# Kernel optimization log

Hardware: AMD Instinct MI355X
Metric: run time of the kernel (lower is better)

## Reference

```python
import jax, jax.numpy as jnp
import numpy as np

B, S, D, A = 8, 4096, 128, 128


def _pos_encoding(seq_len, dim):
    # sin/cos positional encoding, same construction as the torch buffer
    pos = np.arange(seq_len, dtype=np.float32)[:, None]
    div = np.exp(np.arange(0, dim, 2, dtype=np.float32) * (-np.log(10000.0) / dim))
    pe = np.zeros((seq_len, dim), dtype=np.float32)
    pe[:, 0::2] = np.sin(pos * div)
    pe[:, 1::2] = np.cos(pos * div)
    return jnp.asarray(pe)


def setup_inputs() -> dict:
    key = jax.random.key(0)
    ks = jax.random.split(key, 7)
    sc = 1.0 / np.sqrt(D)
    return {
        "x": jax.random.normal(ks[0], (B, S, D), dtype=jnp.float32),
        "Wq": jax.random.normal(ks[1], (D, A), dtype=jnp.float32) * sc,
        "bq": jnp.zeros((A,), dtype=jnp.float32),
        "Wk": jax.random.normal(ks[2], (D, A), dtype=jnp.float32) * sc,
        "bk": jnp.zeros((A,), dtype=jnp.float32),
        "Wv": jax.random.normal(ks[3], (D, A), dtype=jnp.float32) * sc,
        "bv": jnp.zeros((A,), dtype=jnp.float32),
    }


def reference(x, Wq, bq, Wk, bk, Wv, bv):
    b, s, d = x.shape
    pe = _pos_encoding(s, d)  # [S, D]
    xp = x + pe[None]  # broadcast add of positional encoding
    q = xp @ Wq + bq  # [B, S, A]
    k = xp @ Wk + bk
    v = xp @ Wv + bv
    scale = 1.0 / jnp.sqrt(jnp.asarray(Wq.shape[1], dtype=jnp.float32))
    scores = jnp.einsum("bsa,bta->bst", q, k) * scale  # [B, S, S]
    weights = jax.nn.softmax(scores, axis=-1)
    out = jnp.einsum("bst,bta->bsa", weights, v)  # [B, S, A]
    return out
```

## Files before the change

kernel.cpp:

```cpp
#include <hip/hip_runtime.h>

#define BB 8
#define SS 4096
#define DD 128

typedef __attribute__((ext_vector_type(8))) short v8s;
typedef __attribute__((ext_vector_type(4))) float v4f;
typedef __attribute__((ext_vector_type(16))) float v16f;

__device__ __forceinline__ unsigned short f2bf(float f) {
    unsigned int u = __float_as_uint(f);
    u += 0x7fffu + ((u >> 16) & 1u);
    return (unsigned short)(u >> 16);
}
__device__ __forceinline__ unsigned int pk_bf16(float a, float b) {
    unsigned int ua = __float_as_uint(a) + 0x8000u;
    unsigned int ub = __float_as_uint(b) + 0x8000u;
    return __builtin_amdgcn_perm(ub, ua, 0x07060302u);
}

#if !defined(__HIP_DEVICE_COMPILE__)
#define MFMA16(a, b, c) (c)
#define MFMA32(a, b, c) (c)
#define GLDS16(g, l)
#define WAITVM(n)
#define WAITLGKM()
#define BAR()
#else
#define MFMA16(a, b, c) __builtin_amdgcn_mfma_f32_16x16x32_bf16((a), (b), (c), 0, 0, 0)
#define MFMA32(a, b, c) __builtin_amdgcn_mfma_f32_32x32x16_bf16((a), (b), (c), 0, 0, 0)
#define GLDS16(g, l)                                                         \
    __builtin_amdgcn_global_load_lds(                                        \
        (const __attribute__((address_space(1))) unsigned int*)(g),          \
        (__attribute__((address_space(3))) unsigned int*)(l), 16, 0, 0)
#define WAITVM(n) asm volatile("s_waitcnt vmcnt(" #n ")" ::: "memory")
#define WAITLGKM() asm volatile("s_waitcnt lgkmcnt(0)" ::: "memory")
#define BAR()                                                                \
    do {                                                                     \
        asm volatile("" ::: "memory");                                       \
        __builtin_amdgcn_s_barrier();                                        \
        __builtin_amdgcn_sched_barrier(0);                                   \
        asm volatile("" ::: "memory");                                       \
    } while (0)
#endif

#if !defined(__HIP_DEVICE_COMPILE__)
#define EXP2F(x) exp2f(x)
#elif __has_builtin(__builtin_amdgcn_exp2f)
#define EXP2F(x) __builtin_amdgcn_exp2f(x)
#else
#define EXP2F(x) exp2f(x)
#endif

#define QSCALE 0.12751743f

__global__ __launch_bounds__(256) void prep_kernel(
    const float* __restrict__ Wq, const float* __restrict__ Wk,
    const float* __restrict__ Wv, unsigned short* __restrict__ Wt)
{
    int id = blockIdx.x * 256 + threadIdx.x;
    int w = id >> 14;
    int n = (id >> 7) & 127;
    int k = id & 127;
    const float* W = (w == 0) ? Wq : (w == 1) ? Wk : Wv;
    Wt[id] = f2bf(W[k * 128 + n]);
}

__global__ __launch_bounds__(256, 3) void proj_kernel(
    const float* __restrict__ x, const unsigned short* __restrict__ Wt,
    const float* __restrict__ bq, const float* __restrict__ bk,
    const float* __restrict__ bv,
    unsigned short* __restrict__ qo, unsigned short* __restrict__ ko,
    unsigned short* __restrict__ vo)
{
    __shared__ __attribute__((aligned(16))) unsigned short w_lds[128 * 136];
    __shared__ __attribute__((aligned(16))) unsigned short o_lds[9216];

    const int tid = threadIdx.x;
    const int wave = tid >> 6;
    const int lane = tid & 63;
    const int quad = lane >> 4;
    const int l15 = lane & 15;
    const int bid = blockIdx.x;
    const int mat = bid % 3;
    const int rbase = (bid / 3) * 64;

    const unsigned short* Wp = Wt + (mat << 14);
#pragma unroll
    for (int it = 0; it < 8; ++it) {
        int id = it * 256 + tid;
        int n = id >> 4, c8 = id & 15;
        *(v8s*)(w_lds + n * 136 + c8 * 8) = *(const v8s*)(Wp + n * 128 + c8 * 8);
    }

    const int flatrow = rbase + wave * 16 + l15;
    const int srow = flatrow & 4095;
    v8s af[4];
#pragma unroll
    for (int kc = 0; kc < 4; ++kc) {
        const int kbase = kc * 32 + quad * 8;
        const v4f* xp = (const v4f*)(x + (size_t)flatrow * DD + kbase);
        v4f x0 = xp[0], x1 = xp[1];
        float p[8];
#pragma unroll
        for (int j = 0; j < 8; j += 2) {
            float freq = __expf((float)(kbase + j) * -0.07195578415606394f);
            float arg = (float)srow * freq;
            p[j] = __sinf(arg);
            p[j + 1] = __cosf(arg);
        }
        v8s a;
#pragma unroll
        for (int j = 0; j < 4; ++j) a[j] = (short)f2bf(x0[j] + p[j]);
#pragma unroll
        for (int j = 0; j < 4; ++j) a[4 + j] = (short)f2bf(x1[j] + p[4 + j]);
        af[kc] = a;
    }

    const float* bias = (mat == 0) ? bq : (mat == 1) ? bk : bv;
    const int quadp = ((quad & 1) << 1) | (quad >> 1);
    __syncthreads();

#pragma unroll
    for (int nb = 0; nb < 8; ++nb) {
        const int col = nb * 16 + l15;
        v4f acc = {0.f, 0.f, 0.f, 0.f};
#pragma unroll
        for (int kc = 0; kc < 4; ++kc) {
            v8s bf = *(const v8s*)(w_lds + col * 136 + kc * 32 + quad * 8);
            acc = MFMA16(af[kc], bf, acc);
        }
        float bval = bias[col];
#pragma unroll
        for (int reg = 0; reg < 4; ++reg) {
            float val = acc[reg] + bval;
            if (mat == 0) {
                int lr = wave * 16 + quad * 4 + reg;
                o_lds[lr * 136 + col] = f2bf(val * QSCALE);
            } else if (mat == 1) {
                int lr = wave * 16 + quad * 4 + reg;
                o_lds[lr * 136 + col] = f2bf(val);
            } else {
                int plr = wave * 16 + quadp * 4 + reg;
                o_lds[col * 72 + plr] = f2bf(val);
            }
        }
    }
    __syncthreads();

    if (mat <= 1) {
        unsigned short* outp = (mat == 0) ? qo : ko;
#pragma unroll
        for (int it = 0; it < 4; ++it) {
            int id = it * 256 + tid;
            int r = id >> 4, c8 = id & 15;
            *(v8s*)(outp + (size_t)(rbase + r) * DD + c8 * 8) =
                *(const v8s*)(o_lds + r * 136 + c8 * 8);
        }
    } else {
        const int b0 = rbase >> 12, s0 = rbase & 4095;
#pragma unroll
        for (int it = 0; it < 4; ++it) {
            int id = it * 256 + tid;
            int a = id >> 3, c = id & 7;
            *(v8s*)(vo + ((size_t)(b0 * 128 + a)) * SS + s0 + c * 8) =
                *(const v8s*)(o_lds + a * 72 + c * 8);
        }
    }
}

#define HKEYS 2048
#define NT 32
__global__ __launch_bounds__(512, 2) void flash_kernel(
    const unsigned short* __restrict__ qp,
    const unsigned short* __restrict__ kp,
    const unsigned short* __restrict__ vp,
    float* __restrict__ outp)
{
    __shared__ __attribute__((aligned(16))) unsigned short k_lds[2][2][8192];
    __shared__ __attribute__((aligned(16))) unsigned short v_lds[2][2][8192];
    __shared__ float xl[8][32];

    const int tid = threadIdx.x;
    const int wave = tid >> 6;
    const int lane = tid & 63;
    const int hi = lane >> 5;
    const int l31 = lane & 31;
    const int half = wave >> 2;
    const int qs = wave & 3;
    const int wv = wave & 3;
    const int bid = blockIdx.x;
    const int b = bid & 7;
    const int qt = bid >> 3;
    const int qbase = qt * 128;

    const size_t qrow = (size_t)(b * SS + qbase + qs * 32 + l31) * DD;
    v8s qf[8];
#pragma unroll
    for (int kc = 0; kc < 8; ++kc)
        qf[kc] = *(const v8s*)(qp + qrow + kc * 16 + hi * 8);

    v16f o[4];
#pragma unroll
    for (int fg = 0; fg < 4; ++fg)
#pragma unroll
        for (int r = 0; r < 16; ++r) o[fg][r] = 0.f;
    float lp = 0.f;

    const int kro = half * 32768 + l31 * 256 + ((hi ^ (l31 & 15)) << 4);
    const int vro = half * 32768 + l31 * 128 + (((l31 & 7) ^ hi) << 4);

    const int krow = wv * 4 + (lane >> 4);
    const unsigned short* ksrc =
        kp + ((size_t)(b * SS + half * HKEYS) + krow) * DD +
        (((lane & 15) ^ krow) << 3);
    const int vrow = lane >> 3;
    const unsigned short* vsrc =
        vp + (size_t)b * DD * SS + (size_t)(wv * 8 + vrow) * SS + half * HKEYS +
        (((lane & 7) ^ vrow) << 3);
    unsigned short* kd0 = &k_lds[half][0][wv * 512];
    unsigned short* vd0 = &v_lds[half][0][wv * 512];

    auto stage = [&](int p, int t) {
        unsigned short* kd = kd0 + p * 8192;
        unsigned short* vd = vd0 + p * 8192;
        const unsigned short* ks = ksrc + (size_t)t * 64 * DD;
        const unsigned short* vs = vsrc + t * 64;
#pragma unroll
        for (int it = 0; it < 4; ++it)
            GLDS16(ks + (size_t)it * 16 * DD, kd + it * 2048);
#pragma unroll
        for (int it = 0; it < 4; ++it)
            GLDS16(vs + (size_t)it * 32 * SS, vd + it * 2048);
    };

    auto compute = [&](int p, int sub) {
        const int ka = kro + p * 16384 + sub * 8192;
        v16f s;
#pragma unroll
        for (int r = 0; r < 16; ++r) s[r] = 0.f;
#pragma unroll
        for (int kc = 0; kc < 8; ++kc) {
            v8s af = *(const v8s*)((const char*)k_lds + (ka ^ (kc << 5)));
            s = MFMA32(af, qf[kc], s);
        }
        float e[16];
#pragma unroll
        for (int r = 0; r < 16; ++r) e[r] = EXP2F(s[r]);
        lp += (((e[0] + e[1]) + (e[2] + e[3])) + ((e[4] + e[5]) + (e[6] + e[7]))) +
              (((e[8] + e[9]) + (e[10] + e[11])) + ((e[12] + e[13]) + (e[14] + e[15])));
        union { v8s v[2]; unsigned int u[8]; } P;
#pragma unroll
        for (int g = 0; g < 2; ++g)
#pragma unroll
            for (int m = 0; m < 4; ++m)
                P.u[g * 4 + m] = pk_bf16(e[2 * m + 8 * g], e[2 * m + 8 * g + 1]);
        const int vb2 = (vro + p * 16384) ^ (sub << 6);
#pragma unroll
        for (int g = 0; g < 2; ++g) {
            const int vg = vb2 ^ (g << 5);
#pragma unroll
            for (int fg = 0; fg < 4; ++fg) {
                v8s bf = *(const v8s*)((const char*)v_lds + (vg + fg * 4096));
                o[fg] = MFMA32(P.v[g], bf, o[fg]);
            }
        }
    };

    stage(0, 0);
#pragma unroll 1
    for (int t = 0; t < NT; t += 2) {
        stage(1, t + 1);
        WAITVM(8);
        BAR();
        compute(0, 0);
        compute(0, 1);
        WAITLGKM();
        BAR();
        if (t + 2 < NT) {
            stage(0, t + 2);
            WAITVM(8);
        } else {
            WAITVM(0);
        }
        BAR();
        compute(1, 0);
        compute(1, 1);
        WAITLGKM();
        BAR();
    }

    lp += __shfl_xor(lp, 32);
    if (hi == 0) xl[wave][l31] = lp;

    float* kf = (float*)&k_lds[0][0][0];

    auto putO = [&](float* base) {
#pragma unroll
        for (int fg = 0; fg < 4; ++fg) {
            v4f* bp = (v4f*)(base + fg * 1024 + lane * 16);
#pragma unroll
            for (int c = 0; c < 4; ++c) {
                v4f tv = {o[fg][c * 4 + 0], o[fg][c * 4 + 1],
                          o[fg][c * 4 + 2], o[fg][c * 4 + 3]};
                bp[c ^ (lane & 3)] = tv;
            }
        }
    };
    auto addO = [&](const float* base) {
#pragma unroll
        for (int fg = 0; fg < 4; ++fg) {
            const v4f* bp = (const v4f*)(base + fg * 1024 + lane * 16);
#pragma unroll
            for (int c = 0; c < 4; ++c) {
                v4f tv = bp[c ^ (lane & 3)];
#pragma unroll
                for (int j = 0; j < 4; ++j) o[fg][c * 4 + j] += tv[j];
            }
        }
    };

    if (half == 1) putO(kf + qs * 4096);
    __syncthreads();
    if (half == 0) {
        addO(kf + qs * 4096);
        float ir[16];
#pragma unroll
        for (int r = 0; r < 16; ++r) {
            int qr = (r & 3) + 8 * (r >> 2) + 4 * hi;
            ir[r] = 1.0f / (xl[qs][qr] + xl[4 + qs][qr]);
        }
#pragma unroll
        for (int fg = 0; fg < 4; ++fg)
#pragma unroll
            for (int r = 0; r < 16; ++r) {
                int qr = (r & 3) + 8 * (r >> 2) + 4 * hi;
                outp[(size_t)(b * SS + qbase + qs * 32 + qr) * DD +
                     fg * 32 + l31] = o[fg][r] * ir[r];
            }
    }
}

extern "C" void kernel_launch(void* const* d_in, const int* in_sizes, int n_in,
                              void* d_out, int out_size, void* d_ws, size_t ws_size,
                              hipStream_t stream)
{
    const float* x  = (const float*)d_in[0];
    const float* Wq = (const float*)d_in[1];
    const float* bq = (const float*)d_in[2];
    const float* Wk = (const float*)d_in[3];
    const float* bk = (const float*)d_in[4];
    const float* Wv = (const float*)d_in[5];
    const float* bv = (const float*)d_in[6];
    float* out = (float*)d_out;

    unsigned short* Wt = (unsigned short*)d_ws;
    unsigned short* q  = Wt + 49152;
    unsigned short* k  = q + (size_t)BB * SS * DD;
    unsigned short* vT = k + (size_t)BB * SS * DD;

    hipLaunchKernelGGL(prep_kernel, dim3(192), dim3(256), 0, stream,
                       Wq, Wk, Wv, Wt);
    hipLaunchKernelGGL(proj_kernel, dim3(BB * SS / 64 * 3), dim3(256), 0, stream,
                       x, Wt, bq, bk, bv, q, k, vT);
    hipLaunchKernelGGL(flash_kernel, dim3(BB * SS / 128), dim3(512), 0, stream,
                       q, k, vT, out);
}
```

Measured before the change: 167.8 us.

## Store V in MFMA fragment layout and load it straight into registers

The projection kernel now computes Q, K and V in one block per 64 rows, looping over the three weight matrices. This avoids recomputing the positional-encoded input three times. V is written in a fragment-native layout so the flash kernel can load each lane's B operand directly from global memory into registers, double-buffered as X and Y. That removes the V LDS staging and its LDS reads. The cost is more vector registers and global-load latency exposed inside the compute loop, and the projection kernel runs with lower occupancy.

```diff
diff --git a/kernel.cpp b/kernel.cpp
--- a/kernel.cpp
+++ b/kernel.cpp
@@ -66,12 +66,12 @@
     Wt[id] = f2bf(W[k * 128 + n]);
 }
 
-__global__ __launch_bounds__(256, 3) void proj_kernel(
+__global__ __launch_bounds__(256, 2) void proj_kernel(
     const float* __restrict__ x, const unsigned short* __restrict__ Wt,
     const float* __restrict__ bq, const float* __restrict__ bk,
     const float* __restrict__ bv,
     unsigned short* __restrict__ qo, unsigned short* __restrict__ ko,
-    unsigned short* __restrict__ vo)
+    unsigned short* __restrict__ vF)
 {
     __shared__ __attribute__((aligned(16))) unsigned short w_lds[128 * 136];
     __shared__ __attribute__((aligned(16))) unsigned short o_lds[9216];
@@ -81,17 +81,7 @@
     const int lane = tid & 63;
     const int quad = lane >> 4;
     const int l15 = lane & 15;
-    const int bid = blockIdx.x;
-    const int mat = bid % 3;
-    const int rbase = (bid / 3) * 64;
-
-    const unsigned short* Wp = Wt + (mat << 14);
-#pragma unroll
-    for (int it = 0; it < 8; ++it) {
-        int id = it * 256 + tid;
-        int n = id >> 4, c8 = id & 15;
-        *(v8s*)(w_lds + n * 136 + c8 * 8) = *(const v8s*)(Wp + n * 128 + c8 * 8);
-    }
+    const int rbase = blockIdx.x * 64;
 
     const int flatrow = rbase + wave * 16 + l15;
     const int srow = flatrow & 4095;
@@ -117,54 +107,67 @@
         af[kc] = a;
     }
 
-    const float* bias = (mat == 0) ? bq : (mat == 1) ? bk : bv;
     const int quadp = ((quad & 1) << 1) | (quad >> 1);
-    __syncthreads();
-
-#pragma unroll
-    for (int nb = 0; nb < 8; ++nb) {
-        const int col = nb * 16 + l15;
-        v4f acc = {0.f, 0.f, 0.f, 0.f};
-#pragma unroll
-        for (int kc = 0; kc < 4; ++kc) {
-            v8s bf = *(const v8s*)(w_lds + col * 136 + kc * 32 + quad * 8);
-            acc = MFMA16(af[kc], bf, acc);
-        }
-        float bval = bias[col];
-#pragma unroll
-        for (int reg = 0; reg < 4; ++reg) {
-            float val = acc[reg] + bval;
-            if (mat == 0) {
-                int lr = wave * 16 + quad * 4 + reg;
-                o_lds[lr * 136 + col] = f2bf(val * QSCALE);
-            } else if (mat == 1) {
-                int lr = wave * 16 + quad * 4 + reg;
-                o_lds[lr * 136 + col] = f2bf(val);
-            } else {
-                int plr = wave * 16 + quadp * 4 + reg;
-                o_lds[col * 72 + plr] = f2bf(val);
-            }
-        }
-    }
-    __syncthreads();
-
-    if (mat <= 1) {
-        unsigned short* outp = (mat == 0) ? qo : ko;
-#pragma unroll
-        for (int it = 0; it < 4; ++it) {
+    const int b0 = rbase >> 12, s0 = rbase & 4095;
+    const size_t t0 = (size_t)b0 * 128 + (s0 >> 5);
+
+#pragma unroll 1
+    for (int m = 0; m < 3; ++m) {
+        const float* bias = (m == 0) ? bq : (m == 1) ? bk : bv;
+        __syncthreads();
+        const unsigned short* Wp = Wt + (m << 14);
+#pragma unroll
+        for (int it = 0; it < 8; ++it) {
             int id = it * 256 + tid;
-            int r = id >> 4, c8 = id & 15;
-            *(v8s*)(outp + (size_t)(rbase + r) * DD + c8 * 8) =
-                *(const v8s*)(o_lds + r * 136 + c8 * 8);
-        }
-    } else {
-        const int b0 = rbase >> 12, s0 = rbase & 4095;
-#pragma unroll
-        for (int it = 0; it < 4; ++it) {
-            int id = it * 256 + tid;
-            int a = id >> 3, c = id & 7;
-            *(v8s*)(vo + ((size_t)(b0 * 128 + a)) * SS + s0 + c * 8) =
-                *(const v8s*)(o_lds + a * 72 + c * 8);
+            int n = id >> 4, c8 = id & 15;
+            *(v8s*)(w_lds + n * 136 + c8 * 8) = *(const v8s*)(Wp + n * 128 + c8 * 8);
+        }
+        __syncthreads();
+
+#pragma unroll
+        for (int nb = 0; nb < 8; ++nb) {
+            const int col = nb * 16 + l15;
+            v4f acc = {0.f, 0.f, 0.f, 0.f};
+#pragma unroll
+            for (int kc = 0; kc < 4; ++kc) {
+                v8s bf = *(const v8s*)(w_lds + col * 136 + kc * 32 + quad * 8);
+                acc = MFMA16(af[kc], bf, acc);
+            }
+            float bval = bias[col];
+#pragma unroll
+            for (int reg = 0; reg < 4; ++reg) {
+                float val = acc[reg] + bval;
+                if (m == 0) {
+                    int lr = wave * 16 + quad * 4 + reg;
+                    o_lds[lr * 136 + col] = f2bf(val * QSCALE);
+                } else if (m == 1) {
+                    int lr = wave * 16 + quad * 4 + reg;
+                    o_lds[lr * 136 + col] = f2bf(val);
+                } else {
+                    int plr = wave * 16 + quadp * 4 + reg;
+                    o_lds[col * 72 + plr] = f2bf(val);
+                }
+            }
+        }
+        __syncthreads();
+
+        if (m <= 1) {
+            unsigned short* outp = (m == 0) ? qo : ko;
+#pragma unroll
+            for (int it = 0; it < 4; ++it) {
+                int id = it * 256 + tid;
+                int r = id >> 4, c8 = id & 15;
+                *(v8s*)(outp + (size_t)(rbase + r) * DD + c8 * 8) =
+                    *(const v8s*)(o_lds + r * 136 + c8 * 8);
+            }
+        } else {
+#pragma unroll
+            for (int it = 0; it < 4; ++it) {
+                int id = it * 256 + tid;
+                int c = id >> 7, col = id & 127;
+                *(v8s*)(vF + (((t0 + (c >> 2)) * 4 + (c & 3)) * 128 + col) * 8) =
+                    *(const v8s*)(o_lds + col * 72 + c * 8);
+            }
         }
     }
 }
@@ -174,11 +177,10 @@
 __global__ __launch_bounds__(512, 2) void flash_kernel(
     const unsigned short* __restrict__ qp,
     const unsigned short* __restrict__ kp,
-    const unsigned short* __restrict__ vp,
+    const unsigned short* __restrict__ vF,
     float* __restrict__ outp)
 {
     __shared__ __attribute__((aligned(16))) unsigned short k_lds[2][2][8192];
-    __shared__ __attribute__((aligned(16))) unsigned short v_lds[2][2][8192];
     __shared__ float xl[8][32];
 
     const int tid = threadIdx.x;
@@ -208,33 +210,33 @@
     float lp = 0.f;
 
     const int kro = half * 32768 + l31 * 256 + ((hi ^ (l31 & 15)) << 4);
-    const int vro = half * 32768 + l31 * 128 + (((l31 & 7) ^ hi) << 4);
 
     const int krow = wv * 4 + (lane >> 4);
     const unsigned short* ksrc =
         kp + ((size_t)(b * SS + half * HKEYS) + krow) * DD +
         (((lane & 15) ^ krow) << 3);
-    const int vrow = lane >> 3;
-    const unsigned short* vsrc =
-        vp + (size_t)b * DD * SS + (size_t)(wv * 8 + vrow) * SS + half * HKEYS +
-        (((lane & 7) ^ vrow) << 3);
     unsigned short* kd0 = &k_lds[half][0][wv * 512];
-    unsigned short* vd0 = &v_lds[half][0][wv * 512];
-
+
+    const size_t tbase = ((size_t)(b * 128 + half * 64)) * 4096;
+    const unsigned short* vW = vF + tbase + hi * 1024 + l31 * 8;
+
+    v8s X[8], Y[8];
     auto stage = [&](int p, int t) {
         unsigned short* kd = kd0 + p * 8192;
-        unsigned short* vd = vd0 + p * 8192;
         const unsigned short* ks = ksrc + (size_t)t * 64 * DD;
-        const unsigned short* vs = vsrc + t * 64;
 #pragma unroll
         for (int it = 0; it < 4; ++it)
             GLDS16(ks + (size_t)it * 16 * DD, kd + it * 2048);
-#pragma unroll
-        for (int it = 0; it < 4; ++it)
-            GLDS16(vs + (size_t)it * 32 * SS, vd + it * 2048);
-    };
-
-    auto compute = [&](int p, int sub) {
+    };
+    auto loadV = [&](v8s (&buf)[8], int u) {
+        const unsigned short* p = vW + (size_t)u * 4096;
+#pragma unroll
+        for (int g = 0; g < 2; ++g)
+#pragma unroll
+            for (int fg = 0; fg < 4; ++fg)
+                buf[g * 4 + fg] = *(const v8s*)(p + g * 2048 + fg * 256);
+    };
+    auto compute = [&](int p, int sub, const v8s (&buf)[8]) {
         const int ka = kro + p * 16384 + sub * 8192;
         v16f s;
 #pragma unroll
@@ -255,37 +257,44 @@
 #pragma unroll
             for (int m = 0; m < 4; ++m)
                 P.u[g * 4 + m] = pk_bf16(e[2 * m + 8 * g], e[2 * m + 8 * g + 1]);
-        const int vb2 = (vro + p * 16384) ^ (sub << 6);
-#pragma unroll
-        for (int g = 0; g < 2; ++g) {
-            const int vg = vb2 ^ (g << 5);
-#pragma unroll
-            for (int fg = 0; fg < 4; ++fg) {
-                v8s bf = *(const v8s*)((const char*)v_lds + (vg + fg * 4096));
-                o[fg] = MFMA32(P.v[g], bf, o[fg]);
-            }
-        }
+#pragma unroll
+        for (int g = 0; g < 2; ++g)
+#pragma unroll
+            for (int fg = 0; fg < 4; ++fg)
+                o[fg] = MFMA32(P.v[g], buf[g * 4 + fg], o[fg]);
     };
 
     stage(0, 0);
+    loadV(X, 0);
+    loadV(Y, 1);
 #pragma unroll 1
     for (int t = 0; t < NT; t += 2) {
         stage(1, t + 1);
-        WAITVM(8);
+        WAITVM(12);
         BAR();
-        compute(0, 0);
-        compute(0, 1);
+        compute(0, 0, X);
+        loadV(X, 2 * t + 2);
+        WAITVM(12);
+        compute(0, 1, Y);
+        loadV(Y, 2 * t + 3);
         WAITLGKM();
         BAR();
         if (t + 2 < NT) {
             stage(0, t + 2);
+            WAITVM(12);
+        } else {
             WAITVM(8);
+        }
+        BAR();
+        compute(1, 0, X);
+        if (t + 2 < NT) {
+            loadV(X, 2 * t + 4);
+            WAITVM(12);
         } else {
             WAITVM(0);
         }
-        BAR();
-        compute(1, 0);
-        compute(1, 1);
+        compute(1, 1, Y);
+        if (t + 2 < NT) loadV(Y, 2 * t + 5);
         WAITLGKM();
         BAR();
     }
@@ -357,12 +366,12 @@
     unsigned short* Wt = (unsigned short*)d_ws;
     unsigned short* q  = Wt + 49152;
     unsigned short* k  = q + (size_t)BB * SS * DD;
-    unsigned short* vT = k + (size_t)BB * SS * DD;
+    unsigned short* vF = k + (size_t)BB * SS * DD;
 
     hipLaunchKernelGGL(prep_kernel, dim3(192), dim3(256), 0, stream,
                        Wq, Wk, Wv, Wt);
-    hipLaunchKernelGGL(proj_kernel, dim3(BB * SS / 64 * 3), dim3(256), 0, stream,
-                       x, Wt, bq, bk, bv, q, k, vT);
+    hipLaunchKernelGGL(proj_kernel, dim3(BB * SS / 64), dim3(256), 0, stream,
+                       x, Wt, bq, bk, bv, q, k, vF);
     hipLaunchKernelGGL(flash_kernel, dim3(BB * SS / 128), dim3(512), 0, stream,
-                       q, k, vT, out);
-}
+                       q, k, vF, out);
+}
```

New measurement: 167.9 us. Within noise of the previous version (+0.1%).
